# Optimization experiments

Measured on AMD Instinct MI355X. Metric: run time of the kernel, lower is better.

## Reference

```python
import jax, jax.numpy as jnp
import numpy as np

L0 = 0.05    # base segment length (m)
D = 0.0075   # tendon offset (m)
DS = 0.005   # arclength step (m)
BATCH = 262144
ACT_SCALE = 0.01  # realistic tendon displacement scale (m)
NUM_SEGMENTS = 2


def setup_inputs() -> dict:
    key = jax.random.key(0)
    actions = jax.random.uniform(key, (BATCH, 6), dtype=jnp.float32) * ACT_SCALE
    return {"actions": actions}


def _update_action(a):
    l = L0 + a[:, 0]
    ux = a[:, 2] / -(l * D)
    uy = a[:, 1] / (l * D)
    return l, ux, uy


def _ode_f(y):
    # y: [B, 14] = (r[3], R[9] row-major, ux, uy)
    b = y.shape[0]
    ux, uy = y[:, 12], y[:, 13]
    z = jnp.zeros_like(ux)
    # skew matrix u_hat: [0,0,uy; 0,0,-ux; -uy,ux,0]
    u_hat = jnp.stack([
        jnp.stack([z, z, uy], axis=-1),
        jnp.stack([z, z, -ux], axis=-1),
        jnp.stack([-uy, ux, z], axis=-1),
    ], axis=-2)  # [B,3,3]
    R = y[:, 3:12].reshape(b, 3, 3)
    dr = R[:, :, 2]  # R @ e3
    dR = jnp.einsum('bij,bjk->bik', R, u_hat)
    return jnp.concatenate([dr, dR.reshape(b, 9), jnp.zeros((b, 2), y.dtype)], axis=-1)


def _integrate(y0, n_steps):
    # fixed-step RK4 over the arclength grid (step DS); the curvature is
    # constant along s so RK4 at h=DS matches adaptive dopri5 to high accuracy
    h = DS
    def step(y, _):
        k1 = _ode_f(y)
        k2 = _ode_f(y + 0.5 * h * k1)
        k3 = _ode_f(y + 0.5 * h * k2)
        k4 = _ode_f(y + h * k3)
        y_next = y + (h / 6.0) * (k1 + 2.0 * k2 + 2.0 * k3 + k4)
        return y_next, y_next
    _, ys = jax.lax.scan(step, y0, None, length=n_steps)
    return jnp.concatenate([y0[None], ys], axis=0)  # [T, B, 14]


def _mask(sol_batch, lengths):
    # hold the state constant past each rod's tip: sol[t, i] = sol[min(t, len_i), i]
    T, b = sol_batch.shape[0], sol_batch.shape[1]
    idx = jnp.minimum(jnp.arange(T)[:, None], lengths[None, :])  # [T, B]
    return sol_batch[idx, jnp.arange(b)[None, :], :]


def _num_steps(actions):
    l = L0 + np.asarray(actions[:, 0])
    maxl = float(l.max())
    return len(np.arange(0.0, maxl + DS, DS))


def _forward(actions, T):
    b = actions.shape[0]
    y0 = jnp.concatenate([jnp.zeros(3), jnp.eye(3).reshape(9), jnp.zeros(2)]).astype(actions.dtype)
    y0_batch = jnp.tile(y0[None, :], (b, 1))
    l, ux, uy = _update_action(actions[:, 0:3])
    y0_batch = y0_batch.at[:, 12].set(ux).at[:, 13].set(uy)
    sols = []
    for n in range(NUM_SEGMENTS):
        sol_batch = _integrate(y0_batch, T - 1)
        lengths = jnp.floor(l / DS).astype(jnp.int32)
        sol_masked = _mask(sol_batch, lengths)
        sols.append(sol_masked)
        y0_batch = sol_masked[-1]
        # faithful to original: it re-reads segment n's action here (n*3:(n+1)*3),
        # so segment 1 is integrated with segment 0's curvature again
        l, ux, uy = _update_action(actions[:, n * 3:(n + 1) * 3])
        y0_batch = y0_batch.at[:, 12].set(ux).at[:, 13].set(uy)
    return jnp.concatenate(sols, axis=0)  # [2T, B, 14]


def reference(actions):
    T = _num_steps(actions)
    return _forward(actions, T)
```

## Files before the change

### kernel.cpp

```cpp
#include <hip/hip_runtime.h>


#define C_L0 0.05f
#define C_D  0.0075f
#define C_DS 0.005f
#define NB   256

__device__ __forceinline__ void ode_f(const float* __restrict__ y, float ux, float uy,
                                      float* __restrict__ d) {
    d[0] = y[5];
    d[1] = y[8];
    d[2] = y[11];
#pragma unroll
    for (int i = 0; i < 3; ++i) {
        float Ri0 = y[3 + 3 * i + 0];
        float Ri1 = y[3 + 3 * i + 1];
        float Ri2 = y[3 + 3 * i + 2];
        d[3 + 3 * i + 0] = -uy * Ri2;
        d[3 + 3 * i + 1] =  ux * Ri2;
        d[3 + 3 * i + 2] =  uy * Ri0 - ux * Ri1;
    }
}

__device__ __forceinline__ void rk4_step(float* __restrict__ y, float ux, float uy) {
    const float h = C_DS;
    float k1[12], k2[12], k3[12], k4[12], t[12];
    ode_f(y, ux, uy, k1);
#pragma unroll
    for (int i = 0; i < 12; ++i) t[i] = y[i] + (0.5f * h) * k1[i];
    ode_f(t, ux, uy, k2);
#pragma unroll
    for (int i = 0; i < 12; ++i) t[i] = y[i] + (0.5f * h) * k2[i];
    ode_f(t, ux, uy, k3);
#pragma unroll
    for (int i = 0; i < 12; ++i) t[i] = y[i] + h * k3[i];
    ode_f(t, ux, uy, k4);
    const float c = h / 6.0f;
#pragma unroll
    for (int i = 0; i < 12; ++i)
        y[i] = y[i] + c * (k1[i] + 2.0f * k2[i] + 2.0f * k3[i] + k4[i]);
}

__global__ void __launch_bounds__(NB)
ode_kernel(const float* __restrict__ act, float* __restrict__ out, int B, int T) {
    __shared__ float lds[2][NB * 14];

    const int tid = threadIdx.x;
    const int b   = blockIdx.x * NB + tid;

    const float a0 = act[b * 6 + 0];
    const float a1 = act[b * 6 + 1];
    const float a2 = act[b * 6 + 2];

    const float l  = C_L0 + a0;
    const float ld = l * C_D;
    const float ux = a2 / (-ld);
    const float uy = a1 / ld;
    const int   L  = (int)floorf(l / C_DS);

    float y[12];
    y[0] = 0.f; y[1] = 0.f; y[2] = 0.f;
    y[3] = 1.f; y[4] = 0.f; y[5] = 0.f;
    y[6] = 0.f; y[7] = 1.f; y[8] = 0.f;
    y[9] = 0.f; y[10] = 0.f; y[11] = 1.f;

    int buf = 0;
#pragma unroll
    for (int seg = 0; seg < 2; ++seg) {
        for (int t = 0; t < T; ++t) {
            if (t >= 1 && t <= L) rk4_step(y, ux, uy);

            float2* dst = (float2*)&lds[buf][tid * 14];
            dst[0] = make_float2(y[0],  y[1]);
            dst[1] = make_float2(y[2],  y[3]);
            dst[2] = make_float2(y[4],  y[5]);
            dst[3] = make_float2(y[6],  y[7]);
            dst[4] = make_float2(y[8],  y[9]);
            dst[5] = make_float2(y[10], y[11]);
            dst[6] = make_float2(ux, uy);

            __syncthreads();

            const int row = seg * T + t;
            float4* __restrict__ g =
                (float4*)(out + ((size_t)row * (size_t)B + (size_t)blockIdx.x * NB) * 14);
            const float4* __restrict__ s = (const float4*)lds[buf];
            g[tid +   0] = s[tid +   0];
            g[tid + 256] = s[tid + 256];
            g[tid + 512] = s[tid + 512];
            if (tid < 128) g[tid + 768] = s[tid + 768];

            buf ^= 1;
        }
    }
}

extern "C" void kernel_launch(void* const* d_in, const int* in_sizes, int n_in,
                              void* d_out, int out_size, void* d_ws, size_t ws_size,
                              hipStream_t stream) {
    const float* act = (const float*)d_in[0];
    float* out = (float*)d_out;
    int B = in_sizes[0] / 6;
    int T = out_size / (2 * 14 * B);

    int blocks = B / NB;
    hipLaunchKernelGGL(ode_kernel, dim3(blocks), dim3(NB), 0, stream,
                       act, out, B, T);
}
```

Before: 376.0 us.

## Use per-wavefront LDS staging with nontemporal stores, dropping block barriers

Each wavefront now stages and writes out only its own 64 rods' states, so the block-wide __syncthreads is replaced by a wave-local lgkmcnt wait plus a scheduling barrier. Global stores become nontemporal to avoid polluting caches with the large write-only output, and the output pointer is advanced incrementally per row. This removes cross-wave synchronization stalls in a store-bound kernel. It relies on wave-synchronous LDS visibility and the double buffer to avoid hazards.

Result: no change. 376.2 us (+0.1%).

```diff
diff --git a/kernel.cpp b/kernel.cpp
--- a/kernel.cpp
+++ b/kernel.cpp
@@ -5,6 +5,9 @@
 #define C_D  0.0075f
 #define C_DS 0.005f
 #define NB   256
+
+typedef float f32x4 __attribute__((ext_vector_type(4)));
+typedef float f32x2 __attribute__((ext_vector_type(2)));
 
 __device__ __forceinline__ void ode_f(const float* __restrict__ y, float ux, float uy,
                                       float* __restrict__ d) {
@@ -45,8 +48,10 @@
 ode_kernel(const float* __restrict__ act, float* __restrict__ out, int B, int T) {
     __shared__ float lds[2][NB * 14];
 
-    const int tid = threadIdx.x;
-    const int b   = blockIdx.x * NB + tid;
+    const int tid  = threadIdx.x;
+    const int lane = tid & 63;
+    const int wv   = tid >> 6;
+    const int b    = blockIdx.x * NB + tid;
 
     const float a0 = act[b * 6 + 0];
     const float a1 = act[b * 6 + 1];
@@ -64,32 +69,40 @@
     y[6] = 0.f; y[7] = 1.f; y[8] = 0.f;
     y[9] = 0.f; y[10] = 0.f; y[11] = 1.f;
 
+    f32x4* g = (f32x4*)(out + ((size_t)blockIdx.x * NB + (size_t)wv * 64) * 14);
+    const size_t row_stride4 = (size_t)B * 14 / 4;
+
     int buf = 0;
 #pragma unroll
     for (int seg = 0; seg < 2; ++seg) {
         for (int t = 0; t < T; ++t) {
             if (t >= 1 && t <= L) rk4_step(y, ux, uy);
 
-            float2* dst = (float2*)&lds[buf][tid * 14];
-            dst[0] = make_float2(y[0],  y[1]);
-            dst[1] = make_float2(y[2],  y[3]);
-            dst[2] = make_float2(y[4],  y[5]);
-            dst[3] = make_float2(y[6],  y[7]);
-            dst[4] = make_float2(y[8],  y[9]);
-            dst[5] = make_float2(y[10], y[11]);
-            dst[6] = make_float2(ux, uy);
+            f32x2* dst = (f32x2*)&lds[buf][wv * (64 * 14) + lane * 14];
+            dst[0] = (f32x2){y[0],  y[1]};
+            dst[1] = (f32x2){y[2],  y[3]};
+            dst[2] = (f32x2){y[4],  y[5]};
+            dst[3] = (f32x2){y[6],  y[7]};
+            dst[4] = (f32x2){y[8],  y[9]};
+            dst[5] = (f32x2){y[10], y[11]};
+            dst[6] = (f32x2){ux, uy};
 
-            __syncthreads();
+            asm volatile("s_waitcnt lgkmcnt(0)" ::: "memory");
+            __builtin_amdgcn_sched_barrier(0);
 
-            const int row = seg * T + t;
-            float4* __restrict__ g =
-                (float4*)(out + ((size_t)row * (size_t)B + (size_t)blockIdx.x * NB) * 14);
-            const float4* __restrict__ s = (const float4*)lds[buf];
-            g[tid +   0] = s[tid +   0];
-            g[tid + 256] = s[tid + 256];
-            g[tid + 512] = s[tid + 512];
-            if (tid < 128) g[tid + 768] = s[tid + 768];
+            const f32x4* s = (const f32x4*)&lds[buf][wv * (64 * 14)];
+            f32x4 v0 = s[lane];
+            f32x4 v1 = s[lane + 64];
+            f32x4 v2 = s[lane + 128];
+            __builtin_nontemporal_store(v0, &g[lane]);
+            __builtin_nontemporal_store(v1, &g[lane + 64]);
+            __builtin_nontemporal_store(v2, &g[lane + 128]);
+            if (lane < 32) {
+                f32x4 v3 = s[lane + 192];
+                __builtin_nontemporal_store(v3, &g[lane + 192]);
+            }
 
+            g += row_stride4;
             buf ^= 1;
         }
     }
```
